# Kernel optimization log

Measured on AMD Instinct MI355X. Metric: run time of the kernel, lower is better.

The kernel has to match this reference:

```python
import jax, jax.numpy as jnp
import numpy as np
from jax import lax
from jax.scipy.special import logsumexp

B, T, L = 64, 256, 16          # batch, max words per sent, max chars per word
VC, DC, CH = 100, 50, 100      # char vocab, char emb dim, char cnn hidden
VW, DW = 50000, 300            # word vocab, word emb dim
VF, DF = 20, 20                # feature vocab, feature emb dim
H = 256                        # lstm hidden per direction (word_hidden_dim=512)
LAB = 50                       # label alphabet size
N = LAB + 2                    # +START, +STOP tags (NCRF++-style CRF)
START, STOP = N - 2, N - 1
IN = CH + DW + DF              # lstm input dim = 420


def setup_inputs():
    key = jax.random.key(0)
    k = jax.random.split(key, 16)
    p = 0.1
    # pack_padded_sequence requires lengths sorted descending; max length = T
    lens = jnp.sort(jax.random.randint(k[0], (B,), T // 2, T + 1))[::-1].at[0].set(T)
    mask = jnp.arange(T)[None, :] < lens[:, None]
    return dict(
        batch_word=jax.random.randint(k[1], (B, T), 0, VW),
        batch_features=jax.random.randint(k[2], (B, 1), 0, VF),
        batch_wordlen=lens,
        batch_char=jax.random.randint(k[3], (B * T, L), 0, VC),
        batch_charlen=jnp.full((B * T,), L, dtype=jnp.int32),
        batch_charrecover=jnp.arange(B * T),
        mask=mask,
        batch_label=jax.random.randint(k[4], (B, T), 0, LAB),
        char_emb=jax.random.normal(k[5], (VC, DC)) * p,
        conv_w=jax.random.normal(k[6], (CH, DC, 3)) * p,
        conv_b=jnp.zeros((CH,)),
        word_emb=jax.random.normal(k[7], (VW, DW)) * p,
        feat_emb=jax.random.normal(k[8], (VF, DF)) * p,
        w_ih_f=jax.random.normal(k[9], (4 * H, IN)) * p,
        w_hh_f=jax.random.normal(k[10], (4 * H, H)) * p,
        b_f=jnp.zeros((4 * H,)),
        w_ih_b=jax.random.normal(k[11], (4 * H, IN)) * p,
        w_hh_b=jax.random.normal(k[12], (4 * H, H)) * p,
        b_b=jnp.zeros((4 * H,)),
        proj_w=jax.random.normal(k[13], (N, 2 * H)) * p,
        proj_b=jnp.zeros((N,)),
        transitions=(jax.random.normal(k[14], (N, N)) * p)
            .at[:, START].set(-1e4).at[STOP, :].set(-1e4),
    )


def _lstm_dir(x_tb, m_tb, w_ih, w_hh, b, reverse):
    # x_tb: (T,B,IN), m_tb: (T,B,1) float; masked state update == packed-seq LSTM
    xs = jnp.einsum('tbi,gi->tbg', x_tb, w_ih) + b  # precomputed input proj
    def step(carry, inp):
        h, c = carry
        xt, mt = inp
        g = xt + h @ w_hh.T
        i, f, gg, o = jnp.split(g, 4, axis=-1)  # torch gate order i,f,g,o
        c_new = jax.nn.sigmoid(f) * c + jax.nn.sigmoid(i) * jnp.tanh(gg)
        h_new = jax.nn.sigmoid(o) * jnp.tanh(c_new)
        h = mt * h_new + (1 - mt) * h
        c = mt * c_new + (1 - mt) * c
        return (h, c), h
    init = (jnp.zeros((x_tb.shape[1], H), x_tb.dtype),
            jnp.zeros((x_tb.shape[1], H), x_tb.dtype))
    _, hs = lax.scan(step, init, (xs, m_tb), reverse=reverse)
    return hs  # (T,B,H)


def _emissions(batch_word, batch_features, batch_char, batch_charrecover, mask,
               char_emb, conv_w, conv_b, word_emb, feat_emb,
               w_ih_f, w_hh_f, b_f, w_ih_b, w_hh_b, b_b, proj_w, proj_b):
    maskf = mask.astype(jnp.float32)
    # char CNN (dropout = identity at eval time)
    ce = char_emb[batch_char].transpose(0, 2, 1)                     # (BT,DC,L)
    cc = lax.conv_general_dilated(ce, conv_w, (1,), [(1, 1)],
                                  dimension_numbers=('NCH', 'OIH', 'NCH'))
    cc = cc + conv_b[None, :, None]
    pooled = cc.max(axis=2)[batch_charrecover]                       # recover sort order
    char_feats = pooled.reshape(B, T, CH)
    feat_e = jnp.broadcast_to(feat_emb[batch_features], (B, T, DF))  # repeat_interleave
    x = jnp.concatenate([word_emb[batch_word], char_feats, feat_e], axis=2)
    x_tb, m_tb = x.transpose(1, 0, 2), maskf.T[:, :, None]
    hf = _lstm_dir(x_tb, m_tb, w_ih_f, w_hh_f, b_f, reverse=False)
    hb = _lstm_dir(x_tb, m_tb, w_ih_b, w_hh_b, b_b, reverse=True)
    # pad_packed zeroes padded outputs
    lstm_out = jnp.concatenate([hf, hb], axis=-1).transpose(1, 0, 2) * maskf[:, :, None]
    return lstm_out @ proj_w.T + proj_b                              # (B,T,N)


def _crf(feats, mask, batch_wordlen, batch_label, transitions):
    mb = mask.T[:, :, None]                                          # (T,B,1) bool
    s = feats[:, :, None, :] + transitions[None, None]               # (B,T,N,N): s[b,t,i,j]=feat[b,t,j]+T[i,j]
    st = jnp.moveaxis(s, 1, 0)                                       # (T,B,N,N)
    # ---- forward algorithm: log partition Z ----
    def fwd(a, inp):
        st_t, m = inp
        new = logsumexp(a[:, :, None] + st_t, axis=1)
        return jnp.where(m, new, a), None
    alpha, _ = lax.scan(fwd, st[0][:, START, :], (st[1:], mb[1:]))
    Z = logsumexp(alpha + transitions[:, STOP][None, :], axis=1)
    # ---- gold path score ----
    maskf = mask.astype(feats.dtype)
    emit = jnp.sum(jnp.take_along_axis(feats, batch_label[:, :, None], 2)[..., 0] * maskf, 1)
    tr = jnp.sum(transitions[batch_label[:, :-1], batch_label[:, 1:]] * maskf[:, 1:], 1)
    last_tag = jnp.take_along_axis(batch_label, (batch_wordlen - 1)[:, None], 1)[:, 0]
    gold = emit + tr + transitions[START, batch_label[:, 0]] + transitions[last_tag, STOP]
    loss = jnp.sum(Z - gold)
    # ---- viterbi decode ----
    def vstep(v, inp):
        st_t, m = inp
        cur = v[:, :, None] + st_t
        new, bp = cur.max(axis=1), cur.argmax(axis=1)
        v = jnp.where(m, new, v)
        bp = jnp.where(m, bp, jnp.arange(N)[None, :])  # identity bp on padding
        return v, bp
    v, bps = lax.scan(vstep, st[0][:, START, :], (st[1:], mb[1:]))
    term = v + transitions[:, STOP][None, :]
    best_last = jnp.argmax(term, axis=1)
    def back(tag, bp_t):
        prev = jnp.take_along_axis(bp_t, tag[:, None], 1)[:, 0]
        return prev, prev
    _, early = lax.scan(back, best_last, bps, reverse=True)          # tags for t=0..T-2
    path = jnp.concatenate([early, best_last[None]], 0).T            # (B,T)
    tag_seq = jnp.where(mask, path, 0)
    return loss, tag_seq


def reference(batch_word, batch_features, batch_wordlen, batch_char, batch_charlen,
              batch_charrecover, mask, batch_label,
              char_emb, conv_w, conv_b, word_emb, feat_emb,
              w_ih_f, w_hh_f, b_f, w_ih_b, w_hh_b, b_b, proj_w, proj_b, transitions):
    feats = _emissions(batch_word, batch_features, batch_char, batch_charrecover, mask,
                       char_emb, conv_w, conv_b, word_emb, feat_emb,
                       w_ih_f, w_hh_f, b_f, w_ih_b, w_hh_b, b_b, proj_w, proj_b)
    loss, tag_seq = _crf(feats, mask, batch_wordlen, batch_label, transitions)
    return loss, tag_seq
```

## Files before the change

kernel.cpp:

```cpp
#include <hip/hip_runtime.h>
#include <hip/hip_bf16.h>
#include <math.h>

#define BB 64
#define TT 256
#define LCH 16
#define DC 50
#define CHN 100
#define DW 300
#define DF 20
#define HID 256
#define G4 1024
#define INDIM 420
#define KPAD 448
#define NTAG 52
#define TSTART 50
#define TSTOP 51

static constexpr size_t OFF_POOL  = 0;
static constexpr size_t OFF_XH    = 6553600;
static constexpr size_t OFF_W16F  = 21233664;
static constexpr size_t OFF_W16B  = 22151168;
static constexpr size_t OFF_PW16  = 23068672;
static constexpr size_t OFF_HCAT  = 0;
static constexpr size_t OFF_XSF   = 34078720;
static constexpr size_t OFF_XSB   = 101187584;
static constexpr size_t OFF_FEATS = 168296448;
static constexpr size_t OFF_WPF   = 171704320;
static constexpr size_t OFF_WPB   = 172752896;
static constexpr size_t OFF_LOSSB = 173801472;
static constexpr size_t OFF_CTR   = 173801728;

typedef _Float16 v2h __attribute__((ext_vector_type(2)));
typedef _Float16 f16x8 __attribute__((ext_vector_type(8)));
typedef float f32x4 __attribute__((ext_vector_type(4)));
union UH2 { unsigned u; v2h h; };
__device__ __forceinline__ float fdot2u(unsigned a, unsigned b, float c) {
    UH2 x, y; x.u = a; y.u = b;
    return __builtin_amdgcn_fdot2(x.h, y.h, c, false);
}
__device__ __forceinline__ float dot8(uint4 w, uint4 h, float acc) {
    acc = fdot2u(w.x, h.x, acc);
    acc = fdot2u(w.y, h.y, acc);
    acc = fdot2u(w.z, h.z, acc);
    acc = fdot2u(w.w, h.w, acc);
    return acc;
}
#define KEEPU4(v) asm volatile("" : "+v"((v).x), "+v"((v).y), "+v"((v).z), "+v"((v).w))

__device__ __forceinline__ float sigm(float x) { return 1.0f / (1.0f + expf(-x)); }

#define CHARCNN_BLOCKS 2048
#define PREP_BLOCKS 5760

__device__ __forceinline__ void packh_one(const float* __restrict__ w,
                                          _Float16* __restrict__ wph, int e) {
    int r  = e & 7;
    int j  = (e >> 3) & 255;
    int k8 = (e >> 11) & 7;
    int g  = (e >> 14) & 3;
    int s  = (e >> 16) & 3;
    wph[e] = (_Float16)w[(g * 256 + j) * HID + (s * 64 + k8 * 8 + r)];
}
__device__ __forceinline__ void cvtw_one(const float* __restrict__ w,
                                         _Float16* __restrict__ wh, int e) {
    int row = e / KPAD, k = e % KPAD;
    wh[e] = (k < INDIM) ? (_Float16)w[row * INDIM + k] : (_Float16)0.f;
}

__global__ __launch_bounds__(256) void k_front(const int* __restrict__ bchar,
                                               const float* __restrict__ cemb,
                                               const float* __restrict__ cw,
                                               const float* __restrict__ cb,
                                               float* __restrict__ pooled,
                                               const float* __restrict__ whf,
                                               const float* __restrict__ whb,
                                               const float* __restrict__ wihf,
                                               const float* __restrict__ wihb,
                                               const float* __restrict__ pw,
                                               _Float16* __restrict__ wpf,
                                               _Float16* __restrict__ wpb,
                                               _Float16* __restrict__ wh16f,
                                               _Float16* __restrict__ wh16b,
                                               _Float16* __restrict__ pw16,
                                               unsigned* __restrict__ ctr) {
    __shared__ float cwsh[150][100];
    __shared__ float ET[2][DC][20];
    __shared__ int ids[2][LCH];
    int tid = threadIdx.x;
    if (blockIdx.x >= CHARCNN_BLOCKS) {
        int e = (blockIdx.x - CHARCNN_BLOCKS) * 256 + tid;
        if (e == 0) *ctr = 0u;
        if (e < 262144)                packh_one(whf, wpf, e);
        else if (e < 524288)           packh_one(whb, wpb, e - 262144);
        else if (e < 983040)           cvtw_one(wihf, wh16f, e - 524288);
        else if (e < 1441792)          cvtw_one(wihb, wh16b, e - 983040);
        else if (e < 1474560) {
            int p = e - 1441792;
            int row = p >> 9;
            pw16[p] = (row < NTAG) ? (_Float16)pw[row * 512 + (p & 511)] : (_Float16)0.f;
        }
        return;
    }
    int wbase = blockIdx.x * 8;
    for (int i = tid; i < 15000; i += 256) {
        int c = i / 150, row = i % 150;
        cwsh[row][c] = cw[i];
    }
    int half = tid >> 7, c = tid & 127;
    float bcv = (c < CHN) ? cb[c] : 0.f;
    for (int g = 0; g < 8; g += 2) {
        __syncthreads();
        if (tid < 32) ids[tid >> 4][tid & 15] = bchar[(wbase + g + (tid >> 4)) * LCH + (tid & 15)];
        __syncthreads();
        for (int s2 = tid; s2 < 2 * DC * 18; s2 += 256) {
            int w2 = s2 / 900, rem = s2 % 900;
            int l = rem / DC, d = rem % DC;
            float v = 0.f;
            if (l >= 1 && l <= 16) v = cemb[ids[w2][l - 1] * DC + d];
            ET[w2][d][l] = v;
        }
        __syncthreads();
        if (c < CHN) {
            float acc[16];
#pragma unroll
            for (int l = 0; l < 16; l++) acc[l] = 0.f;
            for (int d = 0; d < DC; d++) {
                float e[18];
                float4 t0 = *(const float4*)&ET[half][d][0];
                float4 t1 = *(const float4*)&ET[half][d][4];
                float4 t2 = *(const float4*)&ET[half][d][8];
                float4 t3 = *(const float4*)&ET[half][d][12];
                e[0]=t0.x; e[1]=t0.y; e[2]=t0.z; e[3]=t0.w;
                e[4]=t1.x; e[5]=t1.y; e[6]=t1.z; e[7]=t1.w;
                e[8]=t2.x; e[9]=t2.y; e[10]=t2.z; e[11]=t2.w;
                e[12]=t3.x; e[13]=t3.y; e[14]=t3.z; e[15]=t3.w;
                e[16]=ET[half][d][16]; e[17]=ET[half][d][17];
                float w0 = cwsh[d * 3 + 0][c];
                float w1 = cwsh[d * 3 + 1][c];
                float w2 = cwsh[d * 3 + 2][c];
#pragma unroll
                for (int l = 0; l < 16; l++)
                    acc[l] += w0 * e[l] + w1 * e[l + 1] + w2 * e[l + 2];
            }
            float m = acc[0];
#pragma unroll
            for (int l = 1; l < 16; l++) m = fmaxf(m, acc[l]);
            pooled[(wbase + g + half) * CHN + c] = m + bcv;
        }
    }
}

__global__ __launch_bounds__(256) void k_concat(const int* __restrict__ word,
                                                const int* __restrict__ featsidx,
                                                const int* __restrict__ recover,
                                                const float* __restrict__ wemb,
                                                const float* __restrict__ femb,
                                                const float* __restrict__ pooled,
                                                _Float16* __restrict__ xh) {
    int tid = threadIdx.x;
    for (int wi = 0; wi < 8; wi++) {
        int w = blockIdx.x * 8 + wi;
        int b = w >> 8;
        int wid = word[w];
        _Float16* xr = xh + (size_t)w * KPAD;
        for (int c = tid; c < DW; c += 256) xr[c] = (_Float16)wemb[(size_t)wid * DW + c];
        int rc = recover[w];
        if (tid < CHN) xr[DW + tid] = (_Float16)pooled[rc * CHN + tid];
        if (tid < DF)  xr[DW + CHN + tid] = (_Float16)femb[featsidx[b] * DF + tid];
        if (tid >= 100 && tid < 100 + (KPAD - INDIM)) xr[INDIM + (tid - 100)] = (_Float16)0.f;
    }
}

__global__ __launch_bounds__(256, 4) void k_gemm16b(const _Float16* __restrict__ A,
                                                    const _Float16* __restrict__ Bf,
                                                    const _Float16* __restrict__ Bb,
                                                    const float* __restrict__ biasf,
                                                    const float* __restrict__ biasb,
                                                    float* __restrict__ Cf,
                                                    float* __restrict__ Cb) {
    __shared__ __align__(16) _Float16 Asl[128 * 72];
    __shared__ __align__(16) _Float16 Bfl[64 * 72];
    __shared__ __align__(16) _Float16 Bbl[64 * 72];
    int tid = threadIdx.x;
    int wv = tid >> 6, l = tid & 63;
    int lm = l & 15, lk = l >> 4;
    int n0 = blockIdx.x * 64, m0 = blockIdx.y * 128;
    f32x4 z = {0.f, 0.f, 0.f, 0.f};
    f32x4 af0 = z, af1 = z, af2 = z, af3 = z;
    f32x4 ag0 = z, ag1 = z, ag2 = z, ag3 = z;
    f32x4 ab0 = z, ab1 = z, ab2 = z, ab3 = z;
    f32x4 ac0 = z, ac1 = z, ac2 = z, ac3 = z;
    int ra_[4], rca_[4];
#pragma unroll
    for (int q = 0; q < 4; q++) { int ch = tid + q * 256; ra_[q] = ch >> 3; rca_[q] = ch & 7; }
    int rb_[2], rcb_[2];
#pragma unroll
    for (int q = 0; q < 2; q++) { int ch = tid + q * 256; rb_[q] = ch >> 3; rcb_[q] = ch & 7; }
    for (int k0 = 0; k0 < KPAD; k0 += 64) {
        uint4 va[4], vbf[2], vbb[2];
#pragma unroll
        for (int q = 0; q < 4; q++)
            va[q] = *(const uint4*)&A[(size_t)(m0 + ra_[q]) * KPAD + k0 + rca_[q] * 8];
#pragma unroll
        for (int q = 0; q < 2; q++) {
            vbf[q] = *(const uint4*)&Bf[(size_t)(n0 + rb_[q]) * KPAD + k0 + rcb_[q] * 8];
            vbb[q] = *(const uint4*)&Bb[(size_t)(n0 + rb_[q]) * KPAD + k0 + rcb_[q] * 8];
        }
        __syncthreads();
#pragma unroll
        for (int q = 0; q < 4; q++)
            ((uint4*)Asl)[ra_[q] * 9 + rca_[q]] = va[q];
#pragma unroll
        for (int q = 0; q < 2; q++) {
            ((uint4*)Bfl)[rb_[q] * 9 + rcb_[q]] = vbf[q];
            ((uint4*)Bbl)[rb_[q] * 9 + rcb_[q]] = vbb[q];
        }
        __syncthreads();
#pragma unroll
        for (int kstep = 0; kstep < 2; kstep++) {
            int kk = kstep * 4 + lk;
            f16x8 a0 = ((const f16x8*)Asl)[(wv * 32 + lm) * 9 + kk];
            f16x8 a1 = ((const f16x8*)Asl)[(wv * 32 + 16 + lm) * 9 + kk];
            f16x8 b0 = ((const f16x8*)Bfl)[(0 * 16 + lm) * 9 + kk];
            f16x8 b1 = ((const f16x8*)Bfl)[(1 * 16 + lm) * 9 + kk];
            f16x8 b2 = ((const f16x8*)Bfl)[(2 * 16 + lm) * 9 + kk];
            f16x8 b3 = ((const f16x8*)Bfl)[(3 * 16 + lm) * 9 + kk];
            f16x8 c0 = ((const f16x8*)Bbl)[(0 * 16 + lm) * 9 + kk];
            f16x8 c1 = ((const f16x8*)Bbl)[(1 * 16 + lm) * 9 + kk];
            f16x8 c2 = ((const f16x8*)Bbl)[(2 * 16 + lm) * 9 + kk];
            f16x8 c3 = ((const f16x8*)Bbl)[(3 * 16 + lm) * 9 + kk];
            af0 = __builtin_amdgcn_mfma_f32_16x16x32_f16(a0, b0, af0, 0, 0, 0);
            af1 = __builtin_amdgcn_mfma_f32_16x16x32_f16(a0, b1, af1, 0, 0, 0);
            af2 = __builtin_amdgcn_mfma_f32_16x16x32_f16(a0, b2, af2, 0, 0, 0);
            af3 = __builtin_amdgcn_mfma_f32_16x16x32_f16(a0, b3, af3, 0, 0, 0);
            ag0 = __builtin_amdgcn_mfma_f32_16x16x32_f16(a1, b0, ag0, 0, 0, 0);
            ag1 = __builtin_amdgcn_mfma_f32_16x16x32_f16(a1, b1, ag1, 0, 0, 0);
            ag2 = __builtin_amdgcn_mfma_f32_16x16x32_f16(a1, b2, ag2, 0, 0, 0);
            ag3 = __builtin_amdgcn_mfma_f32_16x16x32_f16(a1, b3, ag3, 0, 0, 0);
            ab0 = __builtin_amdgcn_mfma_f32_16x16x32_f16(a0, c0, ab0, 0, 0, 0);
            ab1 = __builtin_amdgcn_mfma_f32_16x16x32_f16(a0, c1, ab1, 0, 0, 0);
            ab2 = __builtin_amdgcn_mfma_f32_16x16x32_f16(a0, c2, ab2, 0, 0, 0);
            ab3 = __builtin_amdgcn_mfma_f32_16x16x32_f16(a0, c3, ab3, 0, 0, 0);
            ac0 = __builtin_amdgcn_mfma_f32_16x16x32_f16(a1, c0, ac0, 0, 0, 0);
            ac1 = __builtin_amdgcn_mfma_f32_16x16x32_f16(a1, c1, ac1, 0, 0, 0);
            ac2 = __builtin_amdgcn_mfma_f32_16x16x32_f16(a1, c2, ac2, 0, 0, 0);
            ac3 = __builtin_amdgcn_mfma_f32_16x16x32_f16(a1, c3, ac3, 0, 0, 0);
        }
    }
    f32x4 fa[2][4] = {{af0, af1, af2, af3}, {ag0, ag1, ag2, ag3}};
    f32x4 ba[2][4] = {{ab0, ab1, ab2, ab3}, {ac0, ac1, ac2, ac3}};
#pragma unroll
    for (int mi = 0; mi < 2; mi++) {
        int orow = m0 + wv * 32 + mi * 16 + lk * 4;
#pragma unroll
        for (int jn = 0; jn < 4; jn++) {
            int col = n0 + jn * 16 + lm;
            float bvf = biasf[col], bvb = biasb[col];
#pragma unroll
            for (int r = 0; r < 4; r++) {
                Cf[(size_t)(orow + r) * G4 + col] = fa[mi][jn][r] + bvf;
                Cb[(size_t)(orow + r) * G4 + col] = ba[mi][jn][r] + bvb;
            }
        }
    }
}

__global__ __launch_bounds__(1024, 4) void k_lstm(const float* __restrict__ xs_f,
                                               const float* __restrict__ xs_b,
                                               const _Float16* __restrict__ wh_f,
                                               const _Float16* __restrict__ wh_b,
                                               const int* __restrict__ wlen,
                                               _Float16* __restrict__ hcat) {
    int b = blockIdx.x & 63, d = blockIdx.x >> 6;
    const float* xs = d ? xs_b : xs_f;
    const uint4* wp4 = (const uint4*)(d ? wh_b : wh_f);
    int len = wlen[b];
    __shared__ uint4 olds4[8192];
    __shared__ _Float16 __align__(16) hh[256];
    __shared__ float part[4][4][256];
    int tid = threadIdx.x;
    int j = tid & 255, s = tid >> 8;
    const uint4* pi = wp4 + (size_t)((s * 4 + 0) * 8) * 256 + j;
    const uint4* pf = wp4 + (size_t)((s * 4 + 1) * 8) * 256 + j;
    uint4 wg[8];
    {
        const uint4* pg = wp4 + (size_t)((s * 4 + 2) * 8) * 256 + j;
        const uint4* po = wp4 + (size_t)((s * 4 + 3) * 8) * 256 + j;
#pragma unroll
        for (int k8 = 0; k8 < 8; k8++) {
            wg[k8] = pg[k8 * 256];
            olds4[k8 * 1024 + tid] = po[k8 * 256];
        }
    }
#pragma unroll
    for (int k8 = 0; k8 < 8; k8++) KEEPU4(wg[k8]);
    if (tid < 128) ((unsigned*)hh)[tid] = 0u;
    float c = 0.f;
    const uint4* hsh4 = (const uint4*)hh;
    __syncthreads();
    for (int ss = 0; ss < len; ++ss) {
        int t = d ? (len - 1 - ss) : ss;
        float xv0, xv1, xv2, xv3;
        if (tid < 256) {
            const float* xr = xs + (size_t)(b * TT + t) * G4;
            xv0 = xr[tid];
            xv1 = xr[256 + tid];
            xv2 = xr[512 + tid];
            xv3 = xr[768 + tid];
        }
        asm volatile("" : "+v"(pi), "+v"(pf));
        float a0 = 0.f, a1 = 0.f, a2 = 0.f, a3 = 0.f;
#pragma unroll
        for (int k8 = 0; k8 < 8; k8++) {
            uint4 h4 = hsh4[s * 8 + k8];
            uint4 wi = pi[k8 * 256];
            uint4 wf = pf[k8 * 256];
            uint4 wo = olds4[k8 * 1024 + tid];
            a0 = dot8(wi, h4, a0);
            a1 = dot8(wf, h4, a1);
            a2 = dot8(wg[k8], h4, a2);
            a3 = dot8(wo, h4, a3);
        }
        part[s][0][j] = a0;
        part[s][1][j] = a1;
        part[s][2][j] = a2;
        part[s][3][j] = a3;
        __syncthreads();
        if (tid < 256) {
            float s0 = part[0][0][tid] + part[1][0][tid] + part[2][0][tid] + part[3][0][tid] + xv0;
            float s1 = part[0][1][tid] + part[1][1][tid] + part[2][1][tid] + part[3][1][tid] + xv1;
            float s2 = part[0][2][tid] + part[1][2][tid] + part[2][2][tid] + part[3][2][tid] + xv2;
            float s3 = part[0][3][tid] + part[1][3][tid] + part[2][3][tid] + part[3][3][tid] + xv3;
            float ig = sigm(s0), fg = sigm(s1), zg = tanhf(s2), og = sigm(s3);
            c = fg * c + ig * zg;
            float h = og * tanhf(c);
            _Float16 h16 = (_Float16)h;
            hh[tid] = h16;
            hcat[(size_t)(b * TT + t) * 512 + d * 256 + tid] = h16;
        }
        __syncthreads();
    }
}

__global__ __launch_bounds__(256) void k_projm(const _Float16* __restrict__ A,
                                               const _Float16* __restrict__ Bw,
                                               const float* __restrict__ pb,
                                               float* __restrict__ feats) {
    __shared__ __align__(16) _Float16 Al[8 * 64 * 72];
    __shared__ __align__(16) _Float16 Bl[8 * 64 * 72];
    int tid = threadIdx.x;
    int wv = tid >> 6, l = tid & 63;
    int lm = l & 15, lk = l >> 4;
    int m0 = blockIdx.x * 64;
#pragma unroll
    for (int q = 0; q < 16; q++) {
        int ch = tid + q * 256;
        int r = ch >> 6;
        int rem = ch & 63;
        int cnk = rem >> 3, cc = rem & 7;
        ((uint4*)Al)[(cnk * 64 + r) * 9 + cc] =
            *(const uint4*)&A[(size_t)(m0 + r) * 512 + cnk * 64 + cc * 8];
        ((uint4*)Bl)[(cnk * 64 + r) * 9 + cc] =
            *(const uint4*)&Bw[(size_t)r * 512 + cnk * 64 + cc * 8];
    }
    __syncthreads();
    f32x4 z = {0.f, 0.f, 0.f, 0.f};
    f32x4 ac0 = z, ac1 = z, ac2 = z, ac3 = z;
#pragma unroll
    for (int cnk = 0; cnk < 8; cnk++) {
#pragma unroll
        for (int ks = 0; ks < 2; ks++) {
            int kk = ks * 4 + lk;
            f16x8 a  = ((const f16x8*)Al)[(cnk * 64 + wv * 16 + lm) * 9 + kk];
            f16x8 b0 = ((const f16x8*)Bl)[(cnk * 64 +  0 + lm) * 9 + kk];
            f16x8 b1 = ((const f16x8*)Bl)[(cnk * 64 + 16 + lm) * 9 + kk];
            f16x8 b2 = ((const f16x8*)Bl)[(cnk * 64 + 32 + lm) * 9 + kk];
            f16x8 b3 = ((const f16x8*)Bl)[(cnk * 64 + 48 + lm) * 9 + kk];
            ac0 = __builtin_amdgcn_mfma_f32_16x16x32_f16(a, b0, ac0, 0, 0, 0);
            ac1 = __builtin_amdgcn_mfma_f32_16x16x32_f16(a, b1, ac1, 0, 0, 0);
            ac2 = __builtin_amdgcn_mfma_f32_16x16x32_f16(a, b2, ac2, 0, 0, 0);
            ac3 = __builtin_amdgcn_mfma_f32_16x16x32_f16(a, b3, ac3, 0, 0, 0);
        }
    }
    f32x4 accs[4] = {ac0, ac1, ac2, ac3};
    int orow = m0 + wv * 16 + lk * 4;
#pragma unroll
    for (int jn = 0; jn < 4; jn++) {
        int col = jn * 16 + lm;
        if (col < NTAG) {
            float bv = pb[col];
#pragma unroll
            for (int r = 0; r < 4; r++)
                feats[(size_t)(orow + r) * NTAG + col] = accs[jn][r] + bv;
        }
    }
}

__global__ __launch_bounds__(64) void k_crf(const float* __restrict__ feats,
                                            const float* __restrict__ trans,
                                            const int* __restrict__ wlen,
                                            const int* __restrict__ blabel,
                                            float* __restrict__ lossb,
                                            float* __restrict__ outtags,
                                            unsigned* __restrict__ ctr,
                                            float* __restrict__ out) {
    __shared__ float Tm[NTAG * NTAG];
    __shared__ float st[NTAG];
    __shared__ unsigned char bp[TT - 1][NTAG];
    int bid = blockIdx.x;
    int b = bid & 63;
    bool vit = bid >= BB;
    int j = threadIdx.x;
    for (int s = j; s < NTAG * NTAG; s += 64) Tm[s] = trans[s];
    __builtin_amdgcn_wave_barrier();
    int len = wlen[b];
    const float* fb = feats + (size_t)b * TT * NTAG;
    if (j < NTAG) st[j] = fb[j] + Tm[TSTART * NTAG + j];
    __builtin_amdgcn_wave_barrier();
    if (!vit) {
        float frow = (j < NTAG && len > 1) ? fb[NTAG + j] : 0.f;
        for (int t = 1; t < len; t++) {
            float frow_nxt = (j < NTAG && t + 1 < len) ? fb[(size_t)(t + 1) * NTAG + j] : 0.f;
            float anew = 0.f;
            if (j < NTAG) {
                float ma = -1e30f, mb = -1e30f, mc = -1e30f, md = -1e30f;
                for (int i = 0; i < 13; i++) {
                    ma = fmaxf(ma, st[i]      + Tm[i * NTAG + j]);
                    mb = fmaxf(mb, st[i + 13] + Tm[(i + 13) * NTAG + j]);
                    mc = fmaxf(mc, st[i + 26] + Tm[(i + 26) * NTAG + j]);
                    md = fmaxf(md, st[i + 39] + Tm[(i + 39) * NTAG + j]);
                }
                float m1 = fmaxf(fmaxf(ma, mb), fmaxf(mc, md));
                float sa = 0.f, sb = 0.f, sc = 0.f, sd = 0.f;
                for (int i = 0; i < 13; i++) {
                    sa += __expf(st[i]      + Tm[i * NTAG + j] - m1);
                    sb += __expf(st[i + 13] + Tm[(i + 13) * NTAG + j] - m1);
                    sc += __expf(st[i + 26] + Tm[(i + 26) * NTAG + j] - m1);
                    sd += __expf(st[i + 39] + Tm[(i + 39) * NTAG + j] - m1);
                }
                anew = m1 + __logf((sa + sb) + (sc + sd)) + frow;
            }
            __builtin_amdgcn_wave_barrier();
            if (j < NTAG) st[j] = anew;
            __builtin_amdgcn_wave_barrier();
            frow = frow_nxt;
        }
        float red = (j < NTAG) ? st[j] + Tm[j * NTAG + TSTOP] : -1e30f;
        float m1 = red;
#pragma unroll
        for (int m = 32; m; m >>= 1) m1 = fmaxf(m1, __shfl_xor(m1, m));
        float e = (j < NTAG) ? __expf(red - m1) : 0.f;
        float ssum = e;
#pragma unroll
        for (int m = 32; m; m >>= 1) ssum += __shfl_xor(ssum, m);
        const int* lab = blabel + b * TT;
        float gpart = 0.f;
        for (int t = 1 + j; t < len; t += 64)
            gpart += Tm[lab[t - 1] * NTAG + lab[t]] + fb[(size_t)t * NTAG + lab[t]];
#pragma unroll
        for (int m = 32; m; m >>= 1) gpart += __shfl_xor(gpart, m);
        if (j == 0) {
            float Zg = m1 + __logf(ssum);
            float goldv = Tm[TSTART * NTAG + lab[0]] + fb[lab[0]] + gpart
                        + Tm[lab[len - 1] * NTAG + TSTOP];
            lossb[b] = Zg - goldv;
            __threadfence();
            unsigned old = atomicAdd(ctr, 1u);
            if (old == BB - 1) {
                __threadfence();
                float stot = 0.f;
                for (int i = 0; i < BB; i++) stot += lossb[i];
                out[0] = stot;
            }
        }
    } else {
        float frow = (j < NTAG && len > 1) ? fb[NTAG + j] : 0.f;
        for (int t = 1; t < len; t++) {
            float frow_nxt = (j < NTAG && t + 1 < len) ? fb[(size_t)(t + 1) * NTAG + j] : 0.f;
            float vnew = 0.f;
            int arg = 0;
            if (j < NTAG) {
                float va = -1e30f, vb = -1e30f, vc = -1e30f, vd = -1e30f;
                int ia = 0, ib = 13, ic = 26, id2 = 39;
                for (int i = 0; i < 13; i++) {
                    float s0 = st[i]      + Tm[i * NTAG + j];        if (s0 > va) { va = s0; ia = i; }
                    float s1 = st[i + 13] + Tm[(i + 13) * NTAG + j]; if (s1 > vb) { vb = s1; ib = i + 13; }
                    float s2 = st[i + 26] + Tm[(i + 26) * NTAG + j]; if (s2 > vc) { vc = s2; ic = i + 26; }
                    float s3 = st[i + 39] + Tm[(i + 39) * NTAG + j]; if (s3 > vd) { vd = s3; id2 = i + 39; }
                }
                float vm = va; arg = ia;
                if (vb > vm) { vm = vb; arg = ib; }
                if (vc > vm) { vm = vc; arg = ic; }
                if (vd > vm) { vm = vd; arg = id2; }
                vnew = vm + frow;
            }
            __builtin_amdgcn_wave_barrier();
            if (j < NTAG) {
                st[j] = vnew;
                bp[t - 1][j] = (unsigned char)arg;
            }
            __builtin_amdgcn_wave_barrier();
            frow = frow_nxt;
        }
        if (j == 0) {
            int best = 0;
            float vm = st[0] + Tm[0 * NTAG + TSTOP];
            for (int i = 1; i < NTAG; i++) {
                float v = st[i] + Tm[i * NTAG + TSTOP];
                if (v > vm) { vm = v; best = i; }
            }
            float* ot = outtags + (size_t)b * TT;
            int tag = best;
            ot[len - 1] = (float)tag;
            for (int t = len - 2; t >= 0; t--) {
                tag = bp[t][tag];
                ot[t] = (float)tag;
            }
            for (int t = len; t < TT; t++) ot[t] = 0.f;
        }
    }
}

extern "C" void kernel_launch(void* const* d_in, const int* in_sizes, int n_in,
                              void* d_out, int out_size, void* d_ws, size_t ws_size,
                              hipStream_t stream) {
    const int* batch_word     = (const int*)d_in[0];
    const int* batch_features = (const int*)d_in[1];
    const int* batch_wordlen  = (const int*)d_in[2];
    const int* batch_char     = (const int*)d_in[3];
    const int* batch_recover  = (const int*)d_in[5];
    const int* batch_label    = (const int*)d_in[7];
    const float* char_emb = (const float*)d_in[8];
    const float* conv_w   = (const float*)d_in[9];
    const float* conv_b   = (const float*)d_in[10];
    const float* word_emb = (const float*)d_in[11];
    const float* feat_emb = (const float*)d_in[12];
    const float* w_ih_f   = (const float*)d_in[13];
    const float* w_hh_f   = (const float*)d_in[14];
    const float* b_f      = (const float*)d_in[15];
    const float* w_ih_b   = (const float*)d_in[16];
    const float* w_hh_b   = (const float*)d_in[17];
    const float* b_b      = (const float*)d_in[18];
    const float* proj_w   = (const float*)d_in[19];
    const float* proj_b   = (const float*)d_in[20];
    const float* trans    = (const float*)d_in[21];

    char* ws = (char*)d_ws;
    float* pooled   = (float*)(ws + OFF_POOL);
    _Float16* xh    = (_Float16*)(ws + OFF_XH);
    _Float16* wh16f = (_Float16*)(ws + OFF_W16F);
    _Float16* wh16b = (_Float16*)(ws + OFF_W16B);
    _Float16* pw16  = (_Float16*)(ws + OFF_PW16);
    _Float16* hcat  = (_Float16*)(ws + OFF_HCAT);
    float* xs_f   = (float*)(ws + OFF_XSF);
    float* xs_b   = (float*)(ws + OFF_XSB);
    float* feats  = (float*)(ws + OFF_FEATS);
    _Float16* wh_f = (_Float16*)(ws + OFF_WPF);
    _Float16* wh_b = (_Float16*)(ws + OFF_WPB);
    float* lossb  = (float*)(ws + OFF_LOSSB);
    unsigned* ctr = (unsigned*)(ws + OFF_CTR);

    k_front<<<CHARCNN_BLOCKS + PREP_BLOCKS, 256, 0, stream>>>(
        batch_char, char_emb, conv_w, conv_b, pooled,
        w_hh_f, w_hh_b, w_ih_f, w_ih_b, proj_w,
        wh_f, wh_b, wh16f, wh16b, pw16, ctr);
    k_concat<<<(BB * TT) / 8, 256, 0, stream>>>(batch_word, batch_features, batch_recover,
                                                word_emb, feat_emb, pooled, xh);
    k_gemm16b<<<dim3(G4 / 64, (BB * TT) / 128), 256, 0, stream>>>(xh, wh16f, wh16b,
                                                                  b_f, b_b, xs_f, xs_b);
    k_lstm<<<128, 1024, 0, stream>>>(xs_f, xs_b, wh_f, wh_b, batch_wordlen, hcat);
    k_projm<<<(BB * TT) / 64, 256, 0, stream>>>(hcat, pw16, proj_b, feats);
    k_crf<<<2 * BB, 64, 0, stream>>>(feats, trans, batch_wordlen, batch_label,
                                     lossb, (float*)d_out + 1, ctr, (float*)d_out);
}
```

Baseline: 1.364 ms.

## Store input-projection gates in fp16, vectorize embedding copy, cache CRF scores

The input-projection GEMM now writes its gate pre-activations as fp16 instead of fp32, and the LSTM reads them as fp16. This halves the intermediate's memory traffic. The word-embedding copy now uses float2 loads, and the CRF forward and Viterbi loops compute the score terms once into unrolled register arrays instead of reloading them from shared memory. Storing the gates in fp16 lowers their precision, and the register arrays raise register pressure.

```diff
diff --git a/kernel.cpp b/kernel.cpp
--- a/kernel.cpp
+++ b/kernel.cpp
@@ -164,7 +164,11 @@
         int b = w >> 8;
         int wid = word[w];
         _Float16* xr = xh + (size_t)w * KPAD;
-        for (int c = tid; c < DW; c += 256) xr[c] = (_Float16)wemb[(size_t)wid * DW + c];
+        if (tid < 150) {
+            float2 v = ((const float2*)&wemb[(size_t)wid * DW])[tid];
+            xr[2 * tid]     = (_Float16)v.x;
+            xr[2 * tid + 1] = (_Float16)v.y;
+        }
         int rc = recover[w];
         if (tid < CHN) xr[DW + tid] = (_Float16)pooled[rc * CHN + tid];
         if (tid < DF)  xr[DW + CHN + tid] = (_Float16)femb[featsidx[b] * DF + tid];
@@ -177,8 +181,8 @@
                                                     const _Float16* __restrict__ Bb,
                                                     const float* __restrict__ biasf,
                                                     const float* __restrict__ biasb,
-                                                    float* __restrict__ Cf,
-                                                    float* __restrict__ Cb) {
+                                                    _Float16* __restrict__ Cf,
+                                                    _Float16* __restrict__ Cb) {
     __shared__ __align__(16) _Float16 Asl[128 * 72];
     __shared__ __align__(16) _Float16 Bfl[64 * 72];
     __shared__ __align__(16) _Float16 Bbl[64 * 72];
@@ -259,21 +263,21 @@
             float bvf = biasf[col], bvb = biasb[col];
 #pragma unroll
             for (int r = 0; r < 4; r++) {
-                Cf[(size_t)(orow + r) * G4 + col] = fa[mi][jn][r] + bvf;
-                Cb[(size_t)(orow + r) * G4 + col] = ba[mi][jn][r] + bvb;
-            }
-        }
-    }
-}
-
-__global__ __launch_bounds__(1024, 4) void k_lstm(const float* __restrict__ xs_f,
-                                               const float* __restrict__ xs_b,
+                Cf[(size_t)(orow + r) * G4 + col] = (_Float16)(fa[mi][jn][r] + bvf);
+                Cb[(size_t)(orow + r) * G4 + col] = (_Float16)(ba[mi][jn][r] + bvb);
+            }
+        }
+    }
+}
+
+__global__ __launch_bounds__(1024, 4) void k_lstm(const _Float16* __restrict__ xs_f,
+                                               const _Float16* __restrict__ xs_b,
                                                const _Float16* __restrict__ wh_f,
                                                const _Float16* __restrict__ wh_b,
                                                const int* __restrict__ wlen,
                                                _Float16* __restrict__ hcat) {
     int b = blockIdx.x & 63, d = blockIdx.x >> 6;
-    const float* xs = d ? xs_b : xs_f;
+    const _Float16* xs = d ? xs_b : xs_f;
     const uint4* wp4 = (const uint4*)(d ? wh_b : wh_f);
     int len = wlen[b];
     __shared__ uint4 olds4[8192];
@@ -303,11 +307,11 @@
         int t = d ? (len - 1 - ss) : ss;
         float xv0, xv1, xv2, xv3;
         if (tid < 256) {
-            const float* xr = xs + (size_t)(b * TT + t) * G4;
-            xv0 = xr[tid];
-            xv1 = xr[256 + tid];
-            xv2 = xr[512 + tid];
-            xv3 = xr[768 + tid];
+            const _Float16* xr = xs + (size_t)(b * TT + t) * G4;
+            xv0 = (float)xr[tid];
+            xv1 = (float)xr[256 + tid];
+            xv2 = (float)xr[512 + tid];
+            xv3 = (float)xr[768 + tid];
         }
         asm volatile("" : "+v"(pi), "+v"(pf));
         float a0 = 0.f, a1 = 0.f, a2 = 0.f, a3 = 0.f;
@@ -424,20 +428,27 @@
             float frow_nxt = (j < NTAG && t + 1 < len) ? fb[(size_t)(t + 1) * NTAG + j] : 0.f;
             float anew = 0.f;
             if (j < NTAG) {
+                float v0[13], v1[13], v2[13], v3[13];
                 float ma = -1e30f, mb = -1e30f, mc = -1e30f, md = -1e30f;
+#pragma unroll
                 for (int i = 0; i < 13; i++) {
-                    ma = fmaxf(ma, st[i]      + Tm[i * NTAG + j]);
-                    mb = fmaxf(mb, st[i + 13] + Tm[(i + 13) * NTAG + j]);
-                    mc = fmaxf(mc, st[i + 26] + Tm[(i + 26) * NTAG + j]);
-                    md = fmaxf(md, st[i + 39] + Tm[(i + 39) * NTAG + j]);
+                    v0[i] = st[i]      + Tm[i * NTAG + j];
+                    v1[i] = st[i + 13] + Tm[(i + 13) * NTAG + j];
+                    v2[i] = st[i + 26] + Tm[(i + 26) * NTAG + j];
+                    v3[i] = st[i + 39] + Tm[(i + 39) * NTAG + j];
+                    ma = fmaxf(ma, v0[i]);
+                    mb = fmaxf(mb, v1[i]);
+                    mc = fmaxf(mc, v2[i]);
+                    md = fmaxf(md, v3[i]);
                 }
                 float m1 = fmaxf(fmaxf(ma, mb), fmaxf(mc, md));
                 float sa = 0.f, sb = 0.f, sc = 0.f, sd = 0.f;
+#pragma unroll
                 for (int i = 0; i < 13; i++) {
-                    sa += __expf(st[i]      + Tm[i * NTAG + j] - m1);
-                    sb += __expf(st[i + 13] + Tm[(i + 13) * NTAG + j] - m1);
-                    sc += __expf(st[i + 26] + Tm[(i + 26) * NTAG + j] - m1);
-                    sd += __expf(st[i + 39] + Tm[(i + 39) * NTAG + j] - m1);
+                    sa += __expf(v0[i] - m1);
+                    sb += __expf(v1[i] - m1);
+                    sc += __expf(v2[i] - m1);
+                    sd += __expf(v3[i] - m1);
                 }
                 anew = m1 + __logf((sa + sb) + (sc + sd)) + frow;
             }
@@ -481,13 +492,22 @@
             float vnew = 0.f;
             int arg = 0;
             if (j < NTAG) {
+                float v0[13], v1[13], v2[13], v3[13];
+#pragma unroll
+                for (int i = 0; i < 13; i++) {
+                    v0[i] = st[i]      + Tm[i * NTAG + j];
+                    v1[i] = st[i + 13] + Tm[(i + 13) * NTAG + j];
+                    v2[i] = st[i + 26] + Tm[(i + 26) * NTAG + j];
+                    v3[i] = st[i + 39] + Tm[(i + 39) * NTAG + j];
+                }
                 float va = -1e30f, vb = -1e30f, vc = -1e30f, vd = -1e30f;
                 int ia = 0, ib = 13, ic = 26, id2 = 39;
+#pragma unroll
                 for (int i = 0; i < 13; i++) {
-                    float s0 = st[i]      + Tm[i * NTAG + j];        if (s0 > va) { va = s0; ia = i; }
-                    float s1 = st[i + 13] + Tm[(i + 13) * NTAG + j]; if (s1 > vb) { vb = s1; ib = i + 13; }
-                    float s2 = st[i + 26] + Tm[(i + 26) * NTAG + j]; if (s2 > vc) { vc = s2; ic = i + 26; }
-                    float s3 = st[i + 39] + Tm[(i + 39) * NTAG + j]; if (s3 > vd) { vd = s3; id2 = i + 39; }
+                    if (v0[i] > va) { va = v0[i]; ia = i; }
+                    if (v1[i] > vb) { vb = v1[i]; ib = i + 13; }
+                    if (v2[i] > vc) { vc = v2[i]; ic = i + 26; }
+                    if (v3[i] > vd) { vd = v3[i]; id2 = i + 39; }
                 }
                 float vm = va; arg = ia;
                 if (vb > vm) { vm = vb; arg = ib; }
@@ -553,8 +573,8 @@
     _Float16* wh16b = (_Float16*)(ws + OFF_W16B);
     _Float16* pw16  = (_Float16*)(ws + OFF_PW16);
     _Float16* hcat  = (_Float16*)(ws + OFF_HCAT);
-    float* xs_f   = (float*)(ws + OFF_XSF);
-    float* xs_b   = (float*)(ws + OFF_XSB);
+    _Float16* xs_f  = (_Float16*)(ws + OFF_XSF);
+    _Float16* xs_b  = (_Float16*)(ws + OFF_XSB);
     float* feats  = (float*)(ws + OFF_FEATS);
     _Float16* wh_f = (_Float16*)(ws + OFF_WPF);
     _Float16* wh_b = (_Float16*)(ws + OFF_WPB);
```

Measured after the change: 1.325 ms. 2.9% less time.
